# Kernel tuning notes

Hardware: AMD Instinct MI355X
Metric: run time of the kernel (lower is better)

The kernel has to match this reference:

```python
import jax, jax.numpy as jnp
import numpy as np
import math

B, H, W, CIN = 4, 64, 64, 256
G, C, K = 8, 32, 9
MAX_SCALE = 6.0


def setup_inputs() -> dict:
    key = jax.random.key(0)
    ks = jax.random.split(key, 10)
    s = 0.02
    x = jax.random.normal(ks[0], (B, H, W, CIN), dtype=jnp.float32)
    # linear params stored as [in, out]
    v_w = jax.random.normal(ks[1], (CIN, G * C), dtype=jnp.float32) * s
    v_b = jax.random.normal(ks[2], (G * C,), dtype=jnp.float32) * s
    qd_w = jax.random.normal(ks[3], (CIN, G * K * 2), dtype=jnp.float32) * s
    qd_b = jax.random.normal(ks[4], (G * K * 2,), dtype=jnp.float32) * s
    qs_w = jax.random.normal(ks[5], (CIN, G * K), dtype=jnp.float32) * s  # no bias
    qw_w = jax.random.normal(ks[6], (CIN, G * K), dtype=jnp.float32) * s
    qw_b = jax.random.normal(ks[7], (G * K,), dtype=jnp.float32) * s
    out_w = jax.random.normal(ks[8], (G * C, CIN), dtype=jnp.float32) * s
    out_b = jax.random.normal(ks[9], (CIN,), dtype=jnp.float32) * s
    # deformables_prior: 3x3 grid in [-1,1], meshgrid indexing='xy', stacked (x,y)
    n = int(math.isqrt(K))
    d = np.linspace(-1.0, 1.0, n, dtype=np.float32)
    gx, gy = np.meshgrid(d, d, indexing='xy')
    prior = jnp.asarray(np.stack([gx, gy], axis=-1).reshape(1, 1, 1, 1, K, 2))
    # deformables_scale: per-group inverse-sigmoid of (i+1)/G - 1e-4
    sc = np.array([(i + 1) / G - 1e-4 for i in range(G)], dtype=np.float32)
    dscale = jnp.asarray(np.log(sc / (1.0 - sc)).reshape(1, 1, 1, G, 1, 1))
    return dict(x=x, v_w=v_w, v_b=v_b, qd_w=qd_w, qd_b=qd_b, qs_w=qs_w,
                qw_w=qw_w, qw_b=qw_b, out_w=out_w, out_b=out_b,
                prior=prior, dscale=dscale)


def _dcn_sample(v, deform, weights):
    # v: [B,H,W,G,C]; deform: [B,H,W,G,K,2] pixel offsets (x,y); weights: [B,H,W,G,K]
    b_, h_, w_, g_, c_ = v.shape
    ww = jnp.arange(w_, dtype=v.dtype)[None, None, :, None, None]
    hh = jnp.arange(h_, dtype=v.dtype)[None, :, None, None, None]
    px = ww + deform[..., 0]  # [B,H,W,G,K]
    py = hh + deform[..., 1]
    x0 = jnp.floor(px); y0 = jnp.floor(py)
    wx1 = px - x0; wx0 = 1.0 - wx1
    wy1 = py - y0; wy0 = 1.0 - wy1
    bidx = jnp.arange(b_)[:, None, None, None, None]
    gidx = jnp.arange(g_)[None, None, None, :, None]

    def gather(yi, xi):
        valid = ((yi >= 0) & (yi < h_) & (xi >= 0) & (xi < w_)).astype(v.dtype)
        yc = jnp.clip(yi, 0, h_ - 1).astype(jnp.int32)
        xc = jnp.clip(xi, 0, w_ - 1).astype(jnp.int32)
        return v[bidx, yc, xc, gidx] * valid[..., None]  # [B,H,W,G,K,C]

    samp = (gather(y0, x0) * (wy0 * wx0)[..., None]
            + gather(y0, x0 + 1) * (wy0 * wx1)[..., None]
            + gather(y0 + 1, x0) * (wy1 * wx0)[..., None]
            + gather(y0 + 1, x0 + 1) * (wy1 * wx1)[..., None])
    # weighted sum over kernels -> [B,H,W,G,C]
    return jnp.einsum('bhwgkc,bhwgk->bhwgc', samp, weights)


def reference(x, v_w, v_b, qd_w, qd_b, qs_w, qw_w, qw_b, out_w, out_b, prior, dscale):
    b_, h_, w_, _ = x.shape
    v = (x @ v_w + v_b).reshape(b_, h_, w_, G, C)
    deform = (x @ qd_w + qd_b).reshape(b_, h_, w_, G, K, 2)
    scale = (x @ qs_w).reshape(b_, h_, w_, G, K, 1) + dscale
    deform = (deform + prior) * jax.nn.sigmoid(scale) * MAX_SCALE
    weights = (x @ qw_w + qw_b).reshape(b_, h_, w_, G, K)
    out = _dcn_sample(v, deform, weights)  # [B,H,W,G,C]
    out = out.reshape(b_, h_, w_, G * C)
    return out @ out_w + out_b
```

## Files before the change

### kernel.cpp

```cpp
#include <hip/hip_runtime.h>
#include <hip/hip_fp16.h>

#define NPIX 16384

typedef __attribute__((ext_vector_type(8))) short short8;
typedef __attribute__((ext_vector_type(8))) _Float16 half8;
typedef __attribute__((ext_vector_type(4))) float f32x4;

__device__ __forceinline__ unsigned short f2bf(float f) {
    unsigned u = __float_as_uint(f);
    unsigned r = (u + 0x7fffu + ((u >> 16) & 1u)) >> 16;
    return (unsigned short)r;
}
__device__ __forceinline__ unsigned short f2h_us(float f) {
    union { _Float16 h; unsigned short u; } cv;
    cv.h = (_Float16)f;
    return cv.u;
}
__device__ __forceinline__ unsigned hdup(float f) {
    unsigned short u = f2h_us(f);
    return (unsigned)u | ((unsigned)u << 16);
}
__device__ __forceinline__ unsigned hfma2u(unsigned w, unsigned v, unsigned a) {
    union { unsigned u; __half2 h; } W, V, A, R;
    W.u = w; V.u = v; A.u = a;
    R.h = __hfma2(W.h, V.h, A.h);
    return R.u;
}
__device__ __forceinline__ unsigned hadd2u(unsigned a, unsigned b) {
    union { unsigned u; __half2 h; } A, B, R;
    A.u = a; B.u = b;
    R.h = __hadd2(A.h, B.h);
    return R.u;
}

#define GLOAD16(SRC, DST) \
    __builtin_amdgcn_global_load_lds( \
        (const __attribute__((address_space(1))) unsigned*)(SRC), \
        (__attribute__((address_space(3))) unsigned*)(DST), 16, 0, 0)

__device__ __forceinline__ float wsrc(int k, int n,
    const float* v_w, const float* qd_w, const float* qs_w,
    const float* qw_w, const float* out_w)
{
    if (n < 256) return v_w[k * 256 + n];
    n -= 256;
    if (n < 144) return qd_w[k * 144 + n];
    n -= 144;
    if (n < 72)  return qs_w[k * 72 + n];
    n -= 72;
    if (n < 72)  return qw_w[k * 72 + n];
    n -= 72;
    if (n < 32)  return 0.f;
    return out_w[k * 256 + (n - 32)];
}

__global__ __launch_bounds__(256) void prep_all(
    const float* __restrict__ x, unsigned short* __restrict__ xb,
    const float* __restrict__ v_w, const float* __restrict__ qd_w,
    const float* __restrict__ qs_w, const float* __restrict__ qw_w,
    const float* __restrict__ out_w, const float* __restrict__ qd_b,
    const float* __restrict__ qw_b,
    unsigned short* __restrict__ Wt, float* __restrict__ biasD,
    unsigned short* __restrict__ vpad)
{
    __shared__ float t[64][65];
    const int bid = blockIdx.x;
    const int tid = threadIdx.x;

    if (bid < 2048) {
        const int bb = (bid >> 3) + (bid & 7) * 256;
        const size_t i = (size_t)bb * 256 + tid;
        const float4 v0 = *(const float4*)(x + i * 8);
        const float4 v1 = *(const float4*)(x + i * 8 + 4);
        uint4 pk;
        pk.x = f2bf(v0.x) | ((unsigned)f2bf(v0.y) << 16);
        pk.y = f2bf(v0.z) | ((unsigned)f2bf(v0.w) << 16);
        pk.z = f2bf(v1.x) | ((unsigned)f2bf(v1.y) << 16);
        pk.w = f2bf(v1.z) | ((unsigned)f2bf(v1.w) << 16);
        *(uint4*)(xb + i * 8) = pk;
        return;
    }
    if (bid == 2100) {
        for (int i = tid; i < 320; i += 256) {
            float bv = 0.f;
            if (i < 144)                  bv = qd_b[i];
            else if (i >= 216 && i < 288) bv = qw_b[i - 216];
            biasD[i] = bv;
        }
        for (int i = tid; i < 512; i += 256) vpad[i] = 0;
        return;
    }
    const int tile = bid - 2048;
    const int tn = tile % 13;
    const int tk = tile / 13;
    #pragma unroll
    for (int i = 0; i < 16; ++i) {
        const int idx = tid + i * 256;
        const int r = idx >> 6;
        const int c = idx & 63;
        t[r][c] = wsrc(tk * 64 + r, tn * 64 + c, v_w, qd_w, qs_w, qw_w, out_w);
    }
    __syncthreads();
    const bool asF16 = (tn >= 9);
    #pragma unroll
    for (int i = 0; i < 8; ++i) {
        const int idx = tid + i * 256;
        const int rn = idx >> 5;
        const int cc = idx & 31;
        unsigned pk;
        if (asF16)
            pk = (unsigned)f2h_us(t[cc * 2][rn]) | ((unsigned)f2h_us(t[cc * 2 + 1][rn]) << 16);
        else
            pk = (unsigned)f2bf(t[cc * 2][rn]) | ((unsigned)f2bf(t[cc * 2 + 1][rn]) << 16);
        ((unsigned*)(Wt + (size_t)(tn * 64 + rn) * 256 + tk * 64))[cc] = pk;
    }
}

__global__ __launch_bounds__(256) void gemm_proj(
    const unsigned short* __restrict__ A, const unsigned short* __restrict__ Wt,
    const float* __restrict__ v_b, const float* __restrict__ biasD,
    unsigned short* __restrict__ v_bf, float* __restrict__ proj)
{
    __shared__ unsigned short As[64 * 256];
    __shared__ unsigned short Bs[64 * 256];

    const int tid  = threadIdx.x;
    const int wid  = tid >> 6;
    const int lane = tid & 63;
    const int bx   = blockIdx.x;
    const int tile = (bx >> 3) + (bx & 7) * 32;
    const int row0 = tile * 64;
    const int j    = blockIdx.y;

    const unsigned short* Ab = A  + (size_t)row0 * 256;
    const unsigned short* Bb = Wt + (size_t)(j * 64) * 256;
    const int rl = lane >> 5;
    const int gl = lane & 31;

    #pragma unroll
    for (int it = 0; it < 8; ++it) {
        const int r   = wid * 16 + it * 2 + rl;
        const int gsw = gl ^ (r & 7);
        GLOAD16(Ab + r * 256 + gsw * 8, &As[(wid * 16 + it * 2) * 256]);
        GLOAD16(Bb + r * 256 + gsw * 8, &Bs[(wid * 16 + it * 2) * 256]);
    }
    asm volatile("s_waitcnt vmcnt(0)" ::: "memory");
    __syncthreads();

    f32x4 acc00 = {0,0,0,0}, acc01 = {0,0,0,0};
    f32x4 acc10 = {0,0,0,0}, acc11 = {0,0,0,0};

    const int wr = (wid >> 1) * 32;
    const int wc = (wid & 1) * 32;
    const int fr = lane & 15;
    const int fg = lane >> 4;

    const int ra0 = wr + fr, ra1 = ra0 + 16;
    const int rb0 = wc + fr, rb1 = rb0 + 16;
    const int sa  = ra0 & 7;
    const int sb  = rb0 & 7;

    #pragma unroll
    for (int t = 0; t < 8; ++t) {
        const int gran = t * 4 + fg;
        short8 a0 = *(const short8*)&As[ra0 * 256 + (gran ^ sa) * 8];
        short8 a1 = *(const short8*)&As[ra1 * 256 + (gran ^ sa) * 8];
        short8 b0 = *(const short8*)&Bs[rb0 * 256 + (gran ^ sb) * 8];
        short8 b1 = *(const short8*)&Bs[rb1 * 256 + (gran ^ sb) * 8];
        acc00 = __builtin_amdgcn_mfma_f32_16x16x32_bf16(a0, b0, acc00, 0, 0, 0);
        acc01 = __builtin_amdgcn_mfma_f32_16x16x32_bf16(a0, b1, acc01, 0, 0, 0);
        acc10 = __builtin_amdgcn_mfma_f32_16x16x32_bf16(a1, b0, acc10, 0, 0, 0);
        acc11 = __builtin_amdgcn_mfma_f32_16x16x32_bf16(a1, b1, acc11, 0, 0, 0);
    }

    if (j < 4) {
        const int colA = j * 64 + wc + fr;
        const int colB = colA + 16;
        const int gA = colA >> 5, cA = colA & 31;
        const int gB = colB >> 5, cB = colB & 31;
        const float biasA = v_b[colA];
        const float biasB = v_b[colB];
        #pragma unroll
        for (int jj = 0; jj < 4; ++jj) {
            const int r0a = row0 + wr + fg * 4 + jj;
            const int r1a = r0a + 16;
            const int b0i = r0a >> 12;
            const int hw0 = r0a & 4095, hw1 = r1a & 4095;
            v_bf[((size_t)(b0i * 8 + gA) * 4096 + hw0) * 32 + cA] = f2h_us(acc00[jj] + biasA);
            v_bf[((size_t)(b0i * 8 + gB) * 4096 + hw0) * 32 + cB] = f2h_us(acc01[jj] + biasB);
            v_bf[((size_t)(b0i * 8 + gA) * 4096 + hw1) * 32 + cA] = f2h_us(acc10[jj] + biasA);
            v_bf[((size_t)(b0i * 8 + gB) * 4096 + hw1) * 32 + cB] = f2h_us(acc11[jj] + biasB);
        }
    } else {
        const int colA = (j - 4) * 64 + wc + fr;
        const int colB = colA + 16;
        const float biasA = biasD[colA];
        const float biasB = biasD[colB];
        #pragma unroll
        for (int jj = 0; jj < 4; ++jj) {
            const int r0a = row0 + wr + fg * 4 + jj;
            const int r1a = r0a + 16;
            proj[(size_t)r0a * 320 + colA] = acc00[jj] + biasA;
            proj[(size_t)r0a * 320 + colB] = acc01[jj] + biasB;
            proj[(size_t)r1a * 320 + colA] = acc10[jj] + biasA;
            proj[(size_t)r1a * 320 + colB] = acc11[jj] + biasB;
        }
    }
}

__global__ __launch_bounds__(256) void gemm_out(
    const unsigned short* __restrict__ A, const unsigned short* __restrict__ WtO,
    const float* __restrict__ bias, float* __restrict__ Y)
{
    __shared__ unsigned short As[64 * 256];
    __shared__ unsigned short Bs[64 * 256];

    const int tid  = threadIdx.x;
    const int wid  = tid >> 6;
    const int lane = tid & 63;
    const int bx   = blockIdx.x;
    const int tile = (bx >> 3) + (bx & 7) * 32;
    const int row0 = tile * 64;
    const int col0 = blockIdx.y * 64;

    const unsigned short* Ab = A   + (size_t)row0 * 256;
    const unsigned short* Bb = WtO + (size_t)col0 * 256;
    const int rl = lane >> 5;
    const int gl = lane & 31;

    #pragma unroll
    for (int it = 0; it < 8; ++it) {
        const int r   = wid * 16 + it * 2 + rl;
        const int gsw = gl ^ (r & 7);
        GLOAD16(Ab + r * 256 + gsw * 8, &As[(wid * 16 + it * 2) * 256]);
        GLOAD16(Bb + r * 256 + gsw * 8, &Bs[(wid * 16 + it * 2) * 256]);
    }
    asm volatile("s_waitcnt vmcnt(0)" ::: "memory");
    __syncthreads();

    f32x4 acc00 = {0,0,0,0}, acc01 = {0,0,0,0};
    f32x4 acc10 = {0,0,0,0}, acc11 = {0,0,0,0};

    const int wr = (wid >> 1) * 32;
    const int wc = (wid & 1) * 32;
    const int fr = lane & 15;
    const int fg = lane >> 4;

    const int ra0 = wr + fr, ra1 = ra0 + 16;
    const int rb0 = wc + fr, rb1 = rb0 + 16;
    const int sa  = ra0 & 7;
    const int sb  = rb0 & 7;

    #pragma unroll
    for (int t = 0; t < 8; ++t) {
        const int gran = t * 4 + fg;
        half8 a0 = *(const half8*)&As[ra0 * 256 + (gran ^ sa) * 8];
        half8 a1 = *(const half8*)&As[ra1 * 256 + (gran ^ sa) * 8];
        half8 b0 = *(const half8*)&Bs[rb0 * 256 + (gran ^ sb) * 8];
        half8 b1 = *(const half8*)&Bs[rb1 * 256 + (gran ^ sb) * 8];
        acc00 = __builtin_amdgcn_mfma_f32_16x16x32_f16(a0, b0, acc00, 0, 0, 0);
        acc01 = __builtin_amdgcn_mfma_f32_16x16x32_f16(a0, b1, acc01, 0, 0, 0);
        acc10 = __builtin_amdgcn_mfma_f32_16x16x32_f16(a1, b0, acc10, 0, 0, 0);
        acc11 = __builtin_amdgcn_mfma_f32_16x16x32_f16(a1, b1, acc11, 0, 0, 0);
    }

    const int colA = col0 + wc + fr;
    const int colB = colA + 16;
    const float biasA = bias[colA];
    const float biasB = bias[colB];
    #pragma unroll
    for (int jj = 0; jj < 4; ++jj) {
        const int r0a = row0 + wr + fg * 4 + jj;
        const int r1a = r0a + 16;
        Y[(size_t)r0a * 256 + colA] = acc00[jj] + biasA;
        Y[(size_t)r0a * 256 + colB] = acc01[jj] + biasB;
        Y[(size_t)r1a * 256 + colA] = acc10[jj] + biasA;
        Y[(size_t)r1a * 256 + colB] = acc11[jj] + biasB;
    }
}

__global__ __launch_bounds__(256) void dcn_sample8(
    const unsigned short* __restrict__ vbuf,
    const float* __restrict__ proj,
    const float* __restrict__ prior,
    const float* __restrict__ dscale,
    unsigned short* __restrict__ mid)
{
    __shared__ int      offs[576 * 2];
    __shared__ unsigned wpk [576 * 4];

    const int tid = threadIdx.x;
    const int bid  = blockIdx.x;
    const int wg   = (bid & 7) * 256 + (bid >> 3);
    const int pix0 = wg * 8;

    for (int it = tid; it < 576; it += 256) {
        const int p   = it / 72;
        const int rem = it - p * 72;
        const int g   = rem / 9;
        const int k   = rem - g * 9;
        const int pix = pix0 + p;
        const int b   = pix >> 12;
        const int hw  = pix & 4095;
        const int h   = hw >> 6, w = hw & 63;

        const float* row = proj + (size_t)pix * 320;
        const float qdx = row[g * 18 + k * 2 + 0];
        const float qdy = row[g * 18 + k * 2 + 1];
        const float s   = row[144 + g * 9 + k] + dscale[g];
        const float wt  = row[216 + g * 9 + k];
        const float sig6 = 6.0f / (1.0f + __expf(-s));
        const float px = (float)w + (qdx + prior[k * 2 + 0]) * sig6;
        const float py = (float)h + (qdy + prior[k * 2 + 1]) * sig6;

        const float x0f = floorf(px), y0f = floorf(py);
        const int ix = (int)x0f, iy = (int)y0f;
        const float wx1 = px - x0f, wx0 = 1.f - wx1;
        const float wy1 = py - y0f, wy0 = 1.f - wy1;
        const int plane = (b * 8 + g) << 12;

        const bool vy0 = (iy >= 0) & (iy < 64);
        const bool vy1 = (iy >= -1) & (iy < 63);
        const bool vx0 = (ix >= 0) & (ix < 64);
        const bool vx1 = (ix >= -1) & (ix < 63);
        const float w00 = (vy0 & vx0) ? wt * wy0 * wx0 : 0.f;
        const float w10 = (vy1 & vx0) ? wt * wy1 * wx0 : 0.f;
        const float w01 = (vy0 & vx1) ? wt * wy0 * wx1 : 0.f;
        const float w11 = (vy1 & vx1) ? wt * wy1 * wx1 : 0.f;
        wpk[it * 4 + 0] = hdup(w00);
        wpk[it * 4 + 1] = hdup(w10);
        wpk[it * 4 + 2] = hdup(w01);
        wpk[it * 4 + 3] = hdup(w11);

        const int xs  = min(max(ix,     -1), 63);
        const int y0c = min(max(iy,      0), 63);
        const int y1c = min(max(iy + 1,  0), 63);
        offs[it * 2 + 0] = (plane + y0c * 64 + xs) * 64;
        offs[it * 2 + 1] = (plane + y1c * 64 + xs) * 64;
    }
    __syncthreads();

    const int p4 = tid >> 6;
    const int g  = (tid >> 3) & 7;
    const int q  = tid & 7;
    const int xh = q >> 2;
    const int qb = q * 16;
    const char* vbb = (const char*)vbuf;

    unsigned aA0=0,aA1=0,aA2=0,aA3=0, aB0=0,aB1=0,aB2=0,aB3=0;
    unsigned bA0=0,bA1=0,bA2=0,bA3=0, bB0=0,bB1=0,bB2=0,bB3=0;
    const int item0a = p4 * 72 + g * 9;
    const int item0b = (p4 + 4) * 72 + g * 9;

    int2  o2a = *(const int2*)&offs[item0a * 2];
    int2  o2b = *(const int2*)&offs[item0b * 2];
    uint2 wpa = *(const uint2*)&wpk[item0a * 4 + xh * 2];
    uint2 wpb = *(const uint2*)&wpk[item0b * 4 + xh * 2];
    uint4 ra0 = *(const uint4*)(vbb + o2a.x + qb);
    uint4 ra1 = *(const uint4*)(vbb + o2a.y + qb);
    uint4 rb0 = *(const uint4*)(vbb + o2b.x + qb);
    uint4 rb1 = *(const uint4*)(vbb + o2b.y + qb);

    #pragma unroll
    for (int k = 0; k < 9; ++k) {
        const uint2 wpa_c = wpa, wpb_c = wpb;
        const uint4 ra0_c = ra0, ra1_c = ra1, rb0_c = rb0, rb1_c = rb1;

        if (k < 8) {
            const int ita = item0a + k + 1;
            const int itb = item0b + k + 1;
            o2a = *(const int2*)&offs[ita * 2];
            o2b = *(const int2*)&offs[itb * 2];
            wpa = *(const uint2*)&wpk[ita * 4 + xh * 2];
            wpb = *(const uint2*)&wpk[itb * 4 + xh * 2];
            ra0 = *(const uint4*)(vbb + o2a.x + qb);
            ra1 = *(const uint4*)(vbb + o2a.y + qb);
            rb0 = *(const uint4*)(vbb + o2b.x + qb);
            rb1 = *(const uint4*)(vbb + o2b.y + qb);
        }

        aA0 = hfma2u(wpa_c.x, ra0_c.x, aA0);
        aA1 = hfma2u(wpa_c.x, ra0_c.y, aA1);
        aA2 = hfma2u(wpa_c.x, ra0_c.z, aA2);
        aA3 = hfma2u(wpa_c.x, ra0_c.w, aA3);
        aB0 = hfma2u(wpa_c.y, ra1_c.x, aB0);
        aB1 = hfma2u(wpa_c.y, ra1_c.y, aB1);
        aB2 = hfma2u(wpa_c.y, ra1_c.z, aB2);
        aB3 = hfma2u(wpa_c.y, ra1_c.w, aB3);
        bA0 = hfma2u(wpb_c.x, rb0_c.x, bA0);
        bA1 = hfma2u(wpb_c.x, rb0_c.y, bA1);
        bA2 = hfma2u(wpb_c.x, rb0_c.z, bA2);
        bA3 = hfma2u(wpb_c.x, rb0_c.w, bA3);
        bB0 = hfma2u(wpb_c.y, rb1_c.x, bB0);
        bB1 = hfma2u(wpb_c.y, rb1_c.y, bB1);
        bB2 = hfma2u(wpb_c.y, rb1_c.z, bB2);
        bB3 = hfma2u(wpb_c.y, rb1_c.w, bB3);
    }

    uint4 oA, oB;
    {
        unsigned c;
        c = hadd2u(aA0, aB0); c = hadd2u(c, (unsigned)__shfl_xor((int)c, 4)); oA.x = c;
        c = hadd2u(aA1, aB1); c = hadd2u(c, (unsigned)__shfl_xor((int)c, 4)); oA.y = c;
        c = hadd2u(aA2, aB2); c = hadd2u(c, (unsigned)__shfl_xor((int)c, 4)); oA.z = c;
        c = hadd2u(aA3, aB3); c = hadd2u(c, (unsigned)__shfl_xor((int)c, 4)); oA.w = c;
        c = hadd2u(bA0, bB0); c = hadd2u(c, (unsigned)__shfl_xor((int)c, 4)); oB.x = c;
        c = hadd2u(bA1, bB1); c = hadd2u(c, (unsigned)__shfl_xor((int)c, 4)); oB.y = c;
        c = hadd2u(bA2, bB2); c = hadd2u(c, (unsigned)__shfl_xor((int)c, 4)); oB.z = c;
        c = hadd2u(bA3, bB3); c = hadd2u(c, (unsigned)__shfl_xor((int)c, 4)); oB.w = c;
    }
    if (xh == 0) {
        const int cq8 = (q & 3) * 8;
        *(uint4*)(mid + (size_t)(pix0 + p4) * 256 + g * 32 + cq8) = oA;
        *(uint4*)(mid + (size_t)(pix0 + p4 + 4) * 256 + g * 32 + cq8) = oB;
    }
}

extern "C" void kernel_launch(void* const* d_in, const int* in_sizes, int n_in,
                              void* d_out, int out_size, void* d_ws, size_t ws_size,
                              hipStream_t stream)
{
    (void)in_sizes; (void)n_in; (void)out_size; (void)ws_size;

    const float* x      = (const float*)d_in[0];
    const float* v_w    = (const float*)d_in[1];
    const float* v_b    = (const float*)d_in[2];
    const float* qd_w   = (const float*)d_in[3];
    const float* qd_b   = (const float*)d_in[4];
    const float* qs_w   = (const float*)d_in[5];
    const float* qw_w   = (const float*)d_in[6];
    const float* qw_b   = (const float*)d_in[7];
    const float* out_w  = (const float*)d_in[8];
    const float* out_b  = (const float*)d_in[9];
    const float* prior  = (const float*)d_in[10];
    const float* dscale = (const float*)d_in[11];
    float* out = (float*)d_out;

    char* ws = (char*)d_ws;
    unsigned short* xb    = (unsigned short*)(ws);
    unsigned short* v_bf  = (unsigned short*)(ws + 8388608);
    unsigned short* vpad  = (unsigned short*)(ws + 16777216);
    float*          proj  = (float*)(ws + 16778240);
    unsigned short* mid   = (unsigned short*)(ws + 37749760);
    unsigned short* Wt    = (unsigned short*)(ws + 46138368);
    float*          biasD = (float*)(ws + 46564352);

    prep_all<<<dim3(2101), dim3(256), 0, stream>>>(x, xb, v_w, qd_w, qs_w, qw_w,
                                                   out_w, qd_b, qw_b, Wt, biasD, vpad);

    gemm_proj<<<dim3(256, 9), dim3(256), 0, stream>>>(xb, Wt, v_b, biasD, v_bf, proj);

    dcn_sample8<<<dim3(NPIX / 8), dim3(256), 0, stream>>>(v_bf, proj, prior, dscale, mid);

    gemm_out<<<dim3(256, 4), dim3(256), 0, stream>>>(mid, Wt + 576 * 256, out_b, out);
}
```

Before: 55.96 us.

## Fuse input and weight bf16 conversion into the projection GEMM kernel

```diff
diff --git a/kernel.cpp b/kernel.cpp
--- a/kernel.cpp
+++ b/kernel.cpp
@@ -39,244 +39,172 @@
         (const __attribute__((address_space(1))) unsigned*)(SRC), \
         (__attribute__((address_space(3))) unsigned*)(DST), 16, 0, 0)
 
-__device__ __forceinline__ float wsrc(int k, int n,
-    const float* v_w, const float* qd_w, const float* qs_w,
-    const float* qw_w, const float* out_w)
-{
-    if (n < 256) return v_w[k * 256 + n];
-    n -= 256;
-    if (n < 144) return qd_w[k * 144 + n];
-    n -= 144;
-    if (n < 72)  return qs_w[k * 72 + n];
-    n -= 72;
-    if (n < 72)  return qw_w[k * 72 + n];
-    n -= 72;
-    if (n < 32)  return 0.f;
-    return out_w[k * 256 + (n - 32)];
-}
-
-__global__ __launch_bounds__(256) void prep_all(
-    const float* __restrict__ x, unsigned short* __restrict__ xb,
+__global__ __launch_bounds__(256) void gemm_proj_full(
+    const float* __restrict__ x,
     const float* __restrict__ v_w, const float* __restrict__ qd_w,
     const float* __restrict__ qs_w, const float* __restrict__ qw_w,
     const float* __restrict__ out_w, const float* __restrict__ qd_b,
-    const float* __restrict__ qw_b,
-    unsigned short* __restrict__ Wt, float* __restrict__ biasD,
-    unsigned short* __restrict__ vpad)
+    const float* __restrict__ qw_b, const float* __restrict__ v_b,
+    unsigned short* __restrict__ Wt,
+    unsigned short* __restrict__ v_bf, float* __restrict__ proj,
+    unsigned short* __restrict__ vpad, unsigned short* __restrict__ xbtail)
 {
-    __shared__ float t[64][65];
-    const int bid = blockIdx.x;
+    __shared__ union {
+        struct { unsigned short As[64 * 256]; unsigned short Bs[64 * 256]; } g;
+        float t[64][65];
+    } sm;
+
+    const int bx  = blockIdx.x;
     const int tid = threadIdx.x;
 
-    if (bid < 2048) {
-        const int bb = (bid >> 3) + (bid & 7) * 256;
-        const size_t i = (size_t)bb * 256 + tid;
-        const float4 v0 = *(const float4*)(x + i * 8);
-        const float4 v1 = *(const float4*)(x + i * 8 + 4);
-        uint4 pk;
-        pk.x = f2bf(v0.x) | ((unsigned)f2bf(v0.y) << 16);
-        pk.y = f2bf(v0.z) | ((unsigned)f2bf(v0.w) << 16);
-        pk.z = f2bf(v1.x) | ((unsigned)f2bf(v1.y) << 16);
-        pk.w = f2bf(v1.z) | ((unsigned)f2bf(v1.w) << 16);
-        *(uint4*)(xb + i * 8) = pk;
+    if (bx >= 768) {
+        if (bx == 784) {
+            for (int i = tid; i < 512; i += 256) { vpad[i] = 0; xbtail[i] = 0; }
+            return;
+        }
+        const int idx = bx - 768;
+        const int tn = 9 + (idx & 3);
+        const int tk = idx >> 2;
+        #pragma unroll
+        for (int i = 0; i < 16; ++i) {
+            const int ii = tid + i * 256;
+            const int r = ii >> 6, c = ii & 63;
+            sm.t[r][c] = out_w[(size_t)(tk * 64 + r) * 256 + (tn * 64 + c - 576)];
+        }
+        __syncthreads();
+        #pragma unroll
+        for (int i = 0; i < 8; ++i) {
+            const int ii = tid + i * 256;
+            const int rn = ii >> 5, cc = ii & 31;
+            const unsigned pk = (unsigned)f2h_us(sm.t[cc * 2][rn])
+                              | ((unsigned)f2h_us(sm.t[cc * 2 + 1][rn]) << 16);
+            ((unsigned*)(Wt + (size_t)(tn * 64 + rn) * 256 + tk * 64))[cc] = pk;
+        }
         return;
     }
-    if (bid == 2100) {
-        for (int i = tid; i < 320; i += 256) {
-            float bv = 0.f;
-            if (i < 144)                  bv = qd_b[i];
-            else if (i >= 216 && i < 288) bv = qw_b[i - 216];
-            biasD[i] = bv;
-        }
-        for (int i = tid; i < 512; i += 256) vpad[i] = 0;
-        return;
-    }
-    const int tile = bid - 2048;
-    const int tn = tile % 13;
-    const int tk = tile / 13;
-    #pragma unroll
-    for (int i = 0; i < 16; ++i) {
-        const int idx = tid + i * 256;
-        const int r = idx >> 6;
-        const int c = idx & 63;
-        t[r][c] = wsrc(tk * 64 + r, tn * 64 + c, v_w, qd_w, qs_w, qw_w, out_w);
-    }
-    __syncthreads();
-    const bool asF16 = (tn >= 9);
-    #pragma unroll
-    for (int i = 0; i < 8; ++i) {
-        const int idx = tid + i * 256;
-        const int rn = idx >> 5;
-        const int cc = idx & 31;
-        unsigned pk;
-        if (asF16)
-            pk = (unsigned)f2h_us(t[cc * 2][rn]) | ((unsigned)f2h_us(t[cc * 2 + 1][rn]) << 16);
-        else
-            pk = (unsigned)f2bf(t[cc * 2][rn]) | ((unsigned)f2bf(t[cc * 2 + 1][rn]) << 16);
-        ((unsigned*)(Wt + (size_t)(tn * 64 + rn) * 256 + tk * 64))[cc] = pk;
-    }
-}
-
-__global__ __launch_bounds__(256) void gemm_proj(
-    const unsigned short* __restrict__ A, const unsigned short* __restrict__ Wt,
-    const float* __restrict__ v_b, const float* __restrict__ biasD,
-    unsigned short* __restrict__ v_bf, float* __restrict__ proj)
-{
-    __shared__ unsigned short As[64 * 256];
-    __shared__ unsigned short Bs[64 * 256];
-
-    const int tid  = threadIdx.x;
+
+    const int jt   = bx >> 8;
+    const int rblk = bx & 255;
+    const int tile = (rblk >> 3) + (rblk & 7) * 32;
+    const int row0 = tile * 64;
     const int wid  = tid >> 6;
     const int lane = tid & 63;
-    const int bx   = blockIdx.x;
-    const int tile = (bx >> 3) + (bx & 7) * 32;
-    const int row0 = tile * 64;
-    const int j    = blockIdx.y;
-
-    const unsigned short* Ab = A  + (size_t)row0 * 256;
-    const unsigned short* Bb = Wt + (size_t)(j * 64) * 256;
-    const int rl = lane >> 5;
-    const int gl = lane & 31;
-
+
+    const float* Ab = x + (size_t)row0 * 256;
     #pragma unroll
     for (int it = 0; it < 8; ++it) {
-        const int r   = wid * 16 + it * 2 + rl;
-        const int gsw = gl ^ (r & 7);
-        GLOAD16(Ab + r * 256 + gsw * 8, &As[(wid * 16 + it * 2) * 256]);
-        GLOAD16(Bb + r * 256 + gsw * 8, &Bs[(wid * 16 + it * 2) * 256]);
-    }
-    asm volatile("s_waitcnt vmcnt(0)" ::: "memory");
-    __syncthreads();
-
-    f32x4 acc00 = {0,0,0,0}, acc01 = {0,0,0,0};
-    f32x4 acc10 = {0,0,0,0}, acc11 = {0,0,0,0};
+        const int idx = tid + it * 256;
+        const int rr  = idx >> 5;
+        const int gg  = idx & 31;
+        const float4 u0 = *(const float4*)(Ab + rr * 256 + gg * 8);
+        const float4 u1 = *(const float4*)(Ab + rr * 256 + gg * 8 + 4);
+        uint4 pk;
+        pk.x = f2bf(u0.x) | ((unsigned)f2bf(u0.y) << 16);
+        pk.y = f2bf(u0.z) | ((unsigned)f2bf(u0.w) << 16);
+        pk.z = f2bf(u1.x) | ((unsigned)f2bf(u1.y) << 16);
+        pk.w = f2bf(u1.z) | ((unsigned)f2bf(u1.w) << 16);
+        *(uint4*)&sm.g.As[rr * 256 + ((gg ^ (rr & 7)) * 8)] = pk;
+    }
 
     const int wr = (wid >> 1) * 32;
     const int wc = (wid & 1) * 32;
     const int fr = lane & 15;
     const int fg = lane >> 4;
-
     const int ra0 = wr + fr, ra1 = ra0 + 16;
     const int rb0 = wc + fr, rb1 = rb0 + 16;
     const int sa  = ra0 & 7;
-    const int sb  = rb0 & 7;
-
-    #pragma unroll
-    for (int t = 0; t < 8; ++t) {
-        const int gran = t * 4 + fg;
-        short8 a0 = *(const short8*)&As[ra0 * 256 + (gran ^ sa) * 8];
-        short8 a1 = *(const short8*)&As[ra1 * 256 + (gran ^ sa) * 8];
-        short8 b0 = *(const short8*)&Bs[rb0 * 256 + (gran ^ sb) * 8];
-        short8 b1 = *(const short8*)&Bs[rb1 * 256 + (gran ^ sb) * 8];
-        acc00 = __builtin_amdgcn_mfma_f32_16x16x32_bf16(a0, b0, acc00, 0, 0, 0);
-        acc01 = __builtin_amdgcn_mfma_f32_16x16x32_bf16(a0, b1, acc01, 0, 0, 0);
-        acc10 = __builtin_amdgcn_mfma_f32_16x16x32_bf16(a1, b0, acc10, 0, 0, 0);
-        acc11 = __builtin_amdgcn_mfma_f32_16x16x32_bf16(a1, b1, acc11, 0, 0, 0);
-    }
-
-    if (j < 4) {
-        const int colA = j * 64 + wc + fr;
-        const int colB = colA + 16;
-        const int gA = colA >> 5, cA = colA & 31;
-        const int gB = colB >> 5, cB = colB & 31;
-        const float biasA = v_b[colA];
-        const float biasB = v_b[colB];
+    const int sbw = rb0 & 7;
+
+    const int bn  = tid & 63;
+    const int bo0 = tid >> 6;
+
+    #pragma unroll 1
+    for (int jj = 0; jj < 3; ++jj) {
+        const int j = jt * 3 + jj;
+        __syncthreads();
+
+        {
+            const int ng = j * 64 + bn;
+            const float* sp = v_w; int stride = 0; bool zcol = false;
+            if (ng < 256)      { sp = v_w + ng;          stride = 256; }
+            else if (ng < 400) { sp = qd_w + (ng - 256); stride = 144; }
+            else if (ng < 472) { sp = qs_w + (ng - 400); stride = 72; }
+            else if (ng < 544) { sp = qw_w + (ng - 472); stride = 72; }
+            else               { zcol = true; }
+            #pragma unroll
+            for (int i = 0; i < 8; ++i) {
+                const int oct = bo0 + i * 4;
+                const int k0  = oct * 8;
+                uint4 pk = make_uint4(0, 0, 0, 0);
+                if (!zcol) {
+                    const float v0 = sp[(size_t)(k0 + 0) * stride];
+                    const float v1 = sp[(size_t)(k0 + 1) * stride];
+                    const float v2 = sp[(size_t)(k0 + 2) * stride];
+                    const float v3 = sp[(size_t)(k0 + 3) * stride];
+                    const float v4 = sp[(size_t)(k0 + 4) * stride];
+                    const float v5 = sp[(size_t)(k0 + 5) * stride];
+                    const float v6 = sp[(size_t)(k0 + 6) * stride];
+                    const float v7 = sp[(size_t)(k0 + 7) * stride];
+                    pk.x = f2bf(v0) | ((unsigned)f2bf(v1) << 16);
+                    pk.y = f2bf(v2) | ((unsigned)f2bf(v3) << 16);
+                    pk.z = f2bf(v4) | ((unsigned)f2bf(v5) << 16);
+                    pk.w = f2bf(v6) | ((unsigned)f2bf(v7) << 16);
+                }
+                *(uint4*)&sm.g.Bs[bn * 256 + ((oct ^ (bn & 7)) * 8)] = pk;
+            }
+        }
+        __syncthreads();
+
+        f32x4 acc00 = {0,0,0,0}, acc01 = {0,0,0,0};
+        f32x4 acc10 = {0,0,0,0}, acc11 = {0,0,0,0};
         #pragma unroll
-        for (int jj = 0; jj < 4; ++jj) {
-            const int r0a = row0 + wr + fg * 4 + jj;
-            const int r1a = r0a + 16;
-            const int b0i = r0a >> 12;
-            const int hw0 = r0a & 4095, hw1 = r1a & 4095;
-            v_bf[((size_t)(b0i * 8 + gA) * 4096 + hw0) * 32 + cA] = f2h_us(acc00[jj] + biasA);
-            v_bf[((size_t)(b0i * 8 + gB) * 4096 + hw0) * 32 + cB] = f2h_us(acc01[jj] + biasB);
-            v_bf[((size_t)(b0i * 8 + gA) * 4096 + hw1) * 32 + cA] = f2h_us(acc10[jj] + biasA);
-            v_bf[((size_t)(b0i * 8 + gB) * 4096 + hw1) * 32 + cB] = f2h_us(acc11[jj] + biasB);
-        }
-    } else {
-        const int colA = (j - 4) * 64 + wc + fr;
-        const int colB = colA + 16;
-        const float biasA = biasD[colA];
-        const float biasB = biasD[colB];
-        #pragma unroll
-        for (int jj = 0; jj < 4; ++jj) {
-            const int r0a = row0 + wr + fg * 4 + jj;
-            const int r1a = r0a + 16;
-            proj[(size_t)r0a * 320 + colA] = acc00[jj] + biasA;
-            proj[(size_t)r0a * 320 + colB] = acc01[jj] + biasB;
-            proj[(size_t)r1a * 320 + colA] = acc10[jj] + biasA;
-            proj[(size_t)r1a * 320 + colB] = acc11[jj] + biasB;
-        }
-    }
-}
-
-__global__ __launch_bounds__(256) void gemm_out(
-    const unsigned short* __restrict__ A, const unsigned short* __restrict__ WtO,
-    const float* __restrict__ bias, float* __restrict__ Y)
-{
-    __shared__ unsigned short As[64 * 256];
-    __shared__ unsigned short Bs[64 * 256];
-
-    const int tid  = threadIdx.x;
-    const int wid  = tid >> 6;
-    const int lane = tid & 63;
-    const int bx   = blockIdx.x;
-    const int tile = (bx >> 3) + (bx & 7) * 32;
-    const int row0 = tile * 64;
-    const int col0 = blockIdx.y * 64;
-
-    const unsigned short* Ab = A   + (size_t)row0 * 256;
-    const unsigned short* Bb = WtO + (size_t)col0 * 256;
-    const int rl = lane >> 5;
-    const int gl = lane & 31;
-
-    #pragma unroll
-    for (int it = 0; it < 8; ++it) {
-        const int r   = wid * 16 + it * 2 + rl;
-        const int gsw = gl ^ (r & 7);
-        GLOAD16(Ab + r * 256 + gsw * 8, &As[(wid * 16 + it * 2) * 256]);
-        GLOAD16(Bb + r * 256 + gsw * 8, &Bs[(wid * 16 + it * 2) * 256]);
-    }
-    asm volatile("s_waitcnt vmcnt(0)" ::: "memory");
-    __syncthreads();
-
-    f32x4 acc00 = {0,0,0,0}, acc01 = {0,0,0,0};
-    f32x4 acc10 = {0,0,0,0}, acc11 = {0,0,0,0};
-
-    const int wr = (wid >> 1) * 32;
-    const int wc = (wid & 1) * 32;
-    const int fr = lane & 15;
-    const int fg = lane >> 4;
-
-    const int ra0 = wr + fr, ra1 = ra0 + 16;
-    const int rb0 = wc + fr, rb1 = rb0 + 16;
-    const int sa  = ra0 & 7;
-    const int sb  = rb0 & 7;
-
-    #pragma unroll
-    for (int t = 0; t < 8; ++t) {
-        const int gran = t * 4 + fg;
-        half8 a0 = *(const half8*)&As[ra0 * 256 + (gran ^ sa) * 8];
-        half8 a1 = *(const half8*)&As[ra1 * 256 + (gran ^ sa) * 8];
-        half8 b0 = *(const half8*)&Bs[rb0 * 256 + (gran ^ sb) * 8];
-        half8 b1 = *(const half8*)&Bs[rb1 * 256 + (gran ^ sb) * 8];
-        acc00 = __builtin_amdgcn_mfma_f32_16x16x32_f16(a0, b0, acc00, 0, 0, 0);
-        acc01 = __builtin_amdgcn_mfma_f32_16x16x32_f16(a0, b1, acc01, 0, 0, 0);
-        acc10 = __builtin_amdgcn_mfma_f32_16x16x32_f16(a1, b0, acc10, 0, 0, 0);
-        acc11 = __builtin_amdgcn_mfma_f32_16x16x32_f16(a1, b1, acc11, 0, 0, 0);
-    }
-
-    const int colA = col0 + wc + fr;
-    const int colB = colA + 16;
-    const float biasA = bias[colA];
-    const float biasB = bias[colB];
-    #pragma unroll
-    for (int jj = 0; jj < 4; ++jj) {
-        const int r0a = row0 + wr + fg * 4 + jj;
-        const int r1a = r0a + 16;
-        Y[(size_t)r0a * 256 + colA] = acc00[jj] + biasA;
-        Y[(size_t)r0a * 256 + colB] = acc01[jj] + biasB;
-        Y[(size_t)r1a * 256 + colA] = acc10[jj] + biasA;
-        Y[(size_t)r1a * 256 + colB] = acc11[jj] + biasB;
+        for (int t = 0; t < 8; ++t) {
+            const int gran = t * 4 + fg;
+            short8 a0 = *(const short8*)&sm.g.As[ra0 * 256 + ((gran ^ sa) * 8)];
+            short8 a1 = *(const short8*)&sm.g.As[ra1 * 256 + ((gran ^ sa) * 8)];
+            short8 b0 = *(const short8*)&sm.g.Bs[rb0 * 256 + ((gran ^ sbw) * 8)];
+            short8 b1 = *(const short8*)&sm.g.Bs[rb1 * 256 + ((gran ^ sbw) * 8)];
+            acc00 = __builtin_amdgcn_mfma_f32_16x16x32_bf16(a0, b0, acc00, 0, 0, 0);
+            acc01 = __builtin_amdgcn_mfma_f32_16x16x32_bf16(a0, b1, acc01, 0, 0, 0);
+            acc10 = __builtin_amdgcn_mfma_f32_16x16x32_bf16(a1, b0, acc10, 0, 0, 0);
+            acc11 = __builtin_amdgcn_mfma_f32_16x16x32_bf16(a1, b1, acc11, 0, 0, 0);
+        }
+
+        if (j < 4) {
+            const int colA = j * 64 + wc + fr;
+            const int colB = colA + 16;
+            const int gA = colA >> 5, cA = colA & 31;
+            const int gB = colB >> 5, cB = colB & 31;
+            const float biasA = v_b[colA];
+            const float biasB = v_b[colB];
+            #pragma unroll
+            for (int q = 0; q < 4; ++q) {
+                const int r0a = row0 + wr + fg * 4 + q;
+                const int r1a = r0a + 16;
+                const int b0i = r0a >> 12;
+                const int hw0 = r0a & 4095, hw1 = r1a & 4095;
+                v_bf[((size_t)(b0i * 8 + gA) * 4096 + hw0) * 32 + cA] = f2h_us(acc00[q] + biasA);
+                v_bf[((size_t)(b0i * 8 + gB) * 4096 + hw0) * 32 + cB] = f2h_us(acc01[q] + biasB);
+                v_bf[((size_t)(b0i * 8 + gA) * 4096 + hw1) * 32 + cA] = f2h_us(acc10[q] + biasA);
+                v_bf[((size_t)(b0i * 8 + gB) * 4096 + hw1) * 32 + cB] = f2h_us(acc11[q] + biasB);
+            }
+        } else {
+            const int colA = (j - 4) * 64 + wc + fr;
+            const int colB = colA + 16;
+            const float biasA = (colA < 144) ? qd_b[colA]
+                               : ((colA >= 216 && colA < 288) ? qw_b[colA - 216] : 0.f);
+            const float biasB = (colB < 144) ? qd_b[colB]
+                               : ((colB >= 216 && colB < 288) ? qw_b[colB - 216] : 0.f);
+            #pragma unroll
+            for (int q = 0; q < 4; ++q) {
+                const int r0a = row0 + wr + fg * 4 + q;
+                const int r1a = r0a + 16;
+                proj[(size_t)r0a * 320 + colA] = acc00[q] + biasA;
+                proj[(size_t)r0a * 320 + colB] = acc01[q] + biasB;
+                proj[(size_t)r1a * 320 + colA] = acc10[q] + biasA;
+                proj[(size_t)r1a * 320 + colB] = acc11[q] + biasB;
+            }
+        }
     }
 }
 
@@ -417,6 +345,77 @@
     }
 }
 
+__global__ __launch_bounds__(256) void gemm_out(
+    const unsigned short* __restrict__ A, const unsigned short* __restrict__ WtO,
+    const float* __restrict__ bias, float* __restrict__ Y)
+{
+    __shared__ unsigned short As[64 * 256];
+    __shared__ unsigned short Bs[64 * 256];
+
+    const int tid  = threadIdx.x;
+    const int wid  = tid >> 6;
+    const int lane = tid & 63;
+    const int bx   = blockIdx.x;
+    const int tile = (bx >> 3) + (bx & 7) * 32;
+    const int row0 = tile * 64;
+    const int col0 = blockIdx.y * 64;
+
+    const unsigned short* Ab = A   + (size_t)row0 * 256;
+    const unsigned short* Bb = WtO + (size_t)col0 * 256;
+    const int rl = lane >> 5;
+    const int gl = lane & 31;
+
+    #pragma unroll
+    for (int it = 0; it < 8; ++it) {
+        const int r   = wid * 16 + it * 2 + rl;
+        const int gsw = gl ^ (r & 7);
+        GLOAD16(Ab + r * 256 + gsw * 8, &As[(wid * 16 + it * 2) * 256]);
+        GLOAD16(Bb + r * 256 + gsw * 8, &Bs[(wid * 16 + it * 2) * 256]);
+    }
+    asm volatile("s_waitcnt vmcnt(0)" ::: "memory");
+    __syncthreads();
+
+    f32x4 acc00 = {0,0,0,0}, acc01 = {0,0,0,0};
+    f32x4 acc10 = {0,0,0,0}, acc11 = {0,0,0,0};
+
+    const int wr = (wid >> 1) * 32;
+    const int wc = (wid & 1) * 32;
+    const int fr = lane & 15;
+    const int fg = lane >> 4;
+
+    const int ra0 = wr + fr, ra1 = ra0 + 16;
+    const int rb0 = wc + fr, rb1 = rb0 + 16;
+    const int sa  = ra0 & 7;
+    const int sb  = rb0 & 7;
+
+    #pragma unroll
+    for (int t = 0; t < 8; ++t) {
+        const int gran = t * 4 + fg;
+        half8 a0 = *(const half8*)&As[ra0 * 256 + (gran ^ sa) * 8];
+        half8 a1 = *(const half8*)&As[ra1 * 256 + (gran ^ sa) * 8];
+        half8 b0 = *(const half8*)&Bs[rb0 * 256 + (gran ^ sb) * 8];
+        half8 b1 = *(const half8*)&Bs[rb1 * 256 + (gran ^ sb) * 8];
+        acc00 = __builtin_amdgcn_mfma_f32_16x16x32_f16(a0, b0, acc00, 0, 0, 0);
+        acc01 = __builtin_amdgcn_mfma_f32_16x16x32_f16(a0, b1, acc01, 0, 0, 0);
+        acc10 = __builtin_amdgcn_mfma_f32_16x16x32_f16(a1, b0, acc10, 0, 0, 0);
+        acc11 = __builtin_amdgcn_mfma_f32_16x16x32_f16(a1, b1, acc11, 0, 0, 0);
+    }
+
+    const int colA = col0 + wc + fr;
+    const int colB = colA + 16;
+    const float biasA = bias[colA];
+    const float biasB = bias[colB];
+    #pragma unroll
+    for (int jj = 0; jj < 4; ++jj) {
+        const int r0a = row0 + wr + fg * 4 + jj;
+        const int r1a = r0a + 16;
+        Y[(size_t)r0a * 256 + colA] = acc00[jj] + biasA;
+        Y[(size_t)r0a * 256 + colB] = acc01[jj] + biasB;
+        Y[(size_t)r1a * 256 + colA] = acc10[jj] + biasA;
+        Y[(size_t)r1a * 256 + colB] = acc11[jj] + biasB;
+    }
+}
+
 extern "C" void kernel_launch(void* const* d_in, const int* in_sizes, int n_in,
                               void* d_out, int out_size, void* d_ws, size_t ws_size,
                               hipStream_t stream)
@@ -438,18 +437,17 @@
     float* out = (float*)d_out;
 
     char* ws = (char*)d_ws;
-    unsigned short* xb    = (unsigned short*)(ws);
+    unsigned short* xdead = (unsigned short*)(ws);
     unsigned short* v_bf  = (unsigned short*)(ws + 8388608);
     unsigned short* vpad  = (unsigned short*)(ws + 16777216);
     float*          proj  = (float*)(ws + 16778240);
     unsigned short* mid   = (unsigned short*)(ws + 37749760);
     unsigned short* Wt    = (unsigned short*)(ws + 46138368);
-    float*          biasD = (float*)(ws + 46564352);
-
-    prep_all<<<dim3(2101), dim3(256), 0, stream>>>(x, xb, v_w, qd_w, qs_w, qw_w,
-                                                   out_w, qd_b, qw_b, Wt, biasD, vpad);
-
-    gemm_proj<<<dim3(256, 9), dim3(256), 0, stream>>>(xb, Wt, v_b, biasD, v_bf, proj);
+    unsigned short* xbtail = xdead + (8388608 / 2) - 512;
+
+    gemm_proj_full<<<dim3(785), dim3(256), 0, stream>>>(
+        x, v_w, qd_w, qs_w, qw_w, out_w, qd_b, qw_b, v_b,
+        Wt, v_bf, proj, vpad, xbtail);
 
     dcn_sample8<<<dim3(NPIX / 8), dim3(256), 0, stream>>>(v_bf, proj, prior, dscale, mid);
 
```

New measurement: 65.23 us. 16.6% more time.
